# Optimization experiments

Measured on AMD Instinct MI355X. Metric: run time of the kernel, lower is better.

## Reference

```python
import math
import jax, jax.numpy as jnp
from jax import lax
import numpy as np

# Defaults of DifferenceOfGaussians
MIN_SIGMA, SIGMA_RATIO, MAX_SIGMA, TRUNCATE = 1.0, 1.2, 10.0, 4.0
K = int(np.log(MAX_SIGMA / MIN_SIGMA) / np.log(SIGMA_RATIO) + 1)  # 13
SIGMAS_NP = np.array([MIN_SIGMA * SIGMA_RATIO ** i for i in range(K + 1)], np.float32)
MAX_RADIUS = int(TRUNCATE * SIGMAS_NP.max() + 0.5)  # 43
THRESHOLD = 0.001
PAD = (3 - 1) // 2  # footprint=3 -> padding 1
MAX_PEAKS = 32768  # fixed cap for jit-compatible nonzero


def _build_pyramid_weight():
    """Replicates GaussianSmoothing kernels (incl. its exp(-(d/(2s))^2) form),
    zero-padded to the common 87x87 support. Shape [K+1, 1, 87, 87] (OIHW)."""
    ksz = 2 * MAX_RADIUS + 1
    W = np.zeros((K + 1, 1, ksz, ksz), np.float32)
    for i, s in enumerate(SIGMAS_NP):
        r = int(TRUNCATE * s + 0.5)
        n = 2 * r + 1
        g = np.arange(n, dtype=np.float32)
        mean = (n - 1) / 2.0
        g1 = (1.0 / (s * math.sqrt(2 * math.pi))) * np.exp(-(((g - mean) / (2.0 * s)) ** 2))
        k2 = np.outer(g1, g1)
        k2 /= k2.sum()
        p = MAX_RADIUS - r
        W[i, 0, p:p + n, p:p + n] = k2
    return jnp.asarray(W)


def setup_inputs() -> dict:
    key = jax.random.key(0)
    x = jax.random.uniform(key, (1, 1, 512, 512), dtype=jnp.float32)
    weight = _build_pyramid_weight()            # [14, 1, 87, 87]
    sigma_list = jnp.asarray(SIGMAS_NP)         # [14]
    return {"x": x, "weight": weight, "sigma_list": sigma_list}


def reference(x, weight, sigma_list):
    # ConstantPad2d(max_radius) then VALID conv -> output spatially == input
    xp = jnp.pad(x, ((0, 0), (0, 0), (MAX_RADIUS, MAX_RADIUS), (MAX_RADIUS, MAX_RADIUS)))
    g = lax.conv_general_dilated(
        xp, weight, window_strides=(1, 1), padding='VALID',
        dimension_numbers=('NCHW', 'OIHW', 'NCHW'))[0]        # [K+1, H, W]
    # DoG stack scaled by sigma: [K, H, W]
    dog = (g[:-1] - g[1:]) * sigma_list[:K][:, None, None]
    # 3D max-pool, kernel 3, stride 1, pad 1 (same shape)
    image_max = lax.reduce_window(dog, -jnp.inf, lax.max,
                                  (3, 3, 3), (1, 1, 1), [(PAD, PAD)] * 3)
    mask = (dog == image_max) & (dog > THRESHOLD)
    # exclude_border: zero out PAD-wide borders along every dim (incl. scale dim)
    mask = mask.at[:PAD].set(False).at[-PAD:].set(False)
    mask = mask.at[:, :PAD].set(False).at[:, -PAD:].set(False)
    mask = mask.at[:, :, :PAD].set(False).at[:, :, -PAD:].set(False)
    # fixed-size nonzero (padded rows have indices (0,0,0); (0,*,*) is always
    # masked out by border exclusion, so real peaks never collide with padding)
    s_idx, y_idx, x_idx = jnp.nonzero(mask, size=MAX_PEAKS, fill_value=0)
    local_maxima = jnp.stack([sigma_list[s_idx],
                              y_idx.astype(jnp.float32),
                              x_idx.astype(jnp.float32)], axis=1)  # [MAX_PEAKS, 3]
    return local_maxima
```

## Files before the change

kernel.cpp:

```cpp
#include <hip/hip_runtime.h>
#include <hip/hip_bf16.h>


#define OFF_H    0
#define OFF_DOG  18350080
#define OFF_BITS 31981568
#define OFF_GCNT 32407552

#define HROWS 640
#define HPAD  43
#define NSIG 13
#define MAXPEAKS 32768

__device__ __forceinline__ void make_w(float s, double sgn, double* wl, int lane) {
    int r = (int)(4.0f * s + 0.5f);
    int n = 2 * r + 1;
    double v0 = 0.0, v1 = 0.0;
    double sd = (double)s;
    if (lane < n) {
        double d = (double)(lane - r), q = d / (2.0 * sd);
        v0 = exp(-q * q);
    }
    if (lane + 64 < n) {
        double d = (double)(lane + 64 - r), q = d / (2.0 * sd);
        v1 = exp(-q * q);
    }
    double part = v0 + v1;
    for (int m = 1; m < 64; m <<= 1) part += __shfl_xor(part, m);
    double inv = sgn / part;
    wl[lane] = v0 * inv;
    if (lane + 64 < 96) wl[lane + 64] = v1 * inv;
}

__global__ __launch_bounds__(256) void hpass(const float* __restrict__ x,
                                             const float* __restrict__ sigma_list,
                                             float* __restrict__ h) {
    const int i = 13 - blockIdx.y;
    const int t = threadIdx.x;
    float s = sigma_list[i];
    int r = (int)(4.0f * s + 0.5f);
    int n = 2 * r + 1;
    int nceil = (n + 15) & ~15;

    __shared__ double wl[96];
    if (t < 64) make_w(s, +1.0, wl, t);

    {
        float* hp = h + i * (HROWS * 512);
        for (int k = t; k < 688; k += 256) {
            int f = blockIdx.x * 688 + k;
            int g = f >> 9, xc = f & 511;
            int row = (g < HPAD) ? g : (g + 512);
            hp[row * 512 + xc] = 0.0f;
        }
    }

    __shared__ float rowp[8][648];
    int y8 = blockIdx.x * 8;
    for (int rr = 0; rr < 8; ++rr)
        for (int k = t; k < 608; k += 256) {
            int gx = k - 43;
            float val = ((unsigned)gx < 512u) ? x[(y8 + rr) * 512 + gx] : 0.0f;
            rowp[rr][k + (k >> 4)] = val;
        }
    __syncthreads();

    int tsub = t & 31, row = t >> 5;
    int xb = tsub * 16;
    int P0 = 43 - r + xb;
    double acc[16], win[16];
#pragma unroll
    for (int j = 0; j < 16; ++j) acc[j] = 0.0;
#pragma unroll
    for (int sl = 0; sl < 16; ++sl) {
        int p = P0 + sl;
        win[sl] = (double)rowp[row][p + (p >> 4)];
    }
    for (int dc = 0; dc < nceil; dc += 16) {
#pragma unroll
        for (int k = 0; k < 16; ++k) {
            double wd = wl[dc + k];
#pragma unroll
            for (int j = 0; j < 16; ++j)
                acc[j] = fma(wd, win[(k + j) & 15], acc[j]);
            int p = P0 + dc + k + 16;
            win[k] = (double)rowp[row][p + (p >> 4)];
        }
    }
    float* hp = h + (i * HROWS + HPAD + y8 + row) * 512 + xb;
#pragma unroll
    for (int j = 0; j < 16; ++j) hp[j] = (float)acc[j];
}

__device__ __forceinline__ void conv_acc(const float* __restrict__ bp,
                                         int nceil, const double* __restrict__ wl,
                                         double (&acc)[16]) {
    double win[16];
#pragma unroll
    for (int sl = 0; sl < 16; ++sl) win[sl] = (double)bp[sl * 512];
    for (int dc = 0; dc < nceil; dc += 16) {
        const float* rp = bp + (dc + 16) * 512;
#pragma unroll
        for (int k = 0; k < 16; ++k) {
            double wd = wl[dc + k];
#pragma unroll
            for (int j = 0; j < 16; ++j)
                acc[j] = fma(wd, win[(k + j) & 15], acc[j]);
            win[k] = (double)rp[k * 512];
        }
    }
}

__global__ __launch_bounds__(64) void vdog(const float* __restrict__ h,
                                           const float* __restrict__ sigma_list,
                                           float* __restrict__ dog) {
    const int di = 12 - blockIdx.z;
    const int lane = threadIdx.x;
    const int x = blockIdx.x * 64 + lane;
    const int y0 = blockIdx.y * 16;
    float s0 = sigma_list[di], s1 = sigma_list[di + 1];
    int r0 = (int)(4.0f * s0 + 0.5f), n0 = 2 * r0 + 1, nc0 = (n0 + 15) & ~15;
    int r1 = (int)(4.0f * s1 + 0.5f), n1 = 2 * r1 + 1, nc1 = (n1 + 15) & ~15;
    __shared__ double wl0[96], wl1[96];
    make_w(s0, +1.0, wl0, lane);
    make_w(s1, -1.0, wl1, lane);
    __syncthreads();
    double acc[16];
#pragma unroll
    for (int j = 0; j < 16; ++j) acc[j] = 0.0;
    const float* hp0 = h + di * (HROWS * 512);
    conv_acc(hp0 + (HPAD + y0 - r0) * 512 + x, nc0, wl0, acc);
    const float* hp1 = hp0 + HROWS * 512;
    conv_acc(hp1 + (HPAD + y0 - r1) * 512 + x, nc1, wl1, acc);
    double sg = (double)s0;
    float* dp = dog + (di * 512 + y0) * 512 + x;
#pragma unroll
    for (int j = 0; j < 16; ++j) dp[j * 512] = (float)(acc[j] * sg);
}

__global__ __launch_bounds__(512) void detect(const float* __restrict__ dog,
                                              unsigned long long* __restrict__ rowbits,
                                              int* __restrict__ gcnt) {
    const int s = blockIdx.y;
    const int y0 = blockIdx.x * 8;
    const int group = s * 64 + blockIdx.x;
    const int t = threadIdx.x;
    const int w = t >> 6, lane = t & 63;

    if (s == 0 || s == 12) {
        if (t < 64) rowbits[(s * 512 + y0 + (t >> 3)) * 8 + (t & 7)] = 0ull;
        if (t == 0) gcnt[group] = 0;
        return;
    }

    float pm[10], vcen[8];
#pragma unroll
    for (int k = 0; k < 8; ++k) vcen[k] = 0.0f;
#pragma unroll
    for (int q = 0; q < 10; ++q) {
        int yy = y0 - 1 + q;
        float m = -3.0e38f;
        if ((unsigned)yy < 512u) {
            float a = dog[((s - 1) * 512 + yy) * 512 + t];
            float b = dog[(s * 512 + yy) * 512 + t];
            float c = dog[((s + 1) * 512 + yy) * 512 + t];
            m = fmaxf(a, fmaxf(b, c));
            if (q >= 1 && q <= 8) vcen[q - 1] = b;
        }
        pm[q] = m;
    }
    __shared__ float cml[8][512];
    __shared__ int cnt[8][8];
#pragma unroll
    for (int k = 0; k < 8; ++k)
        cml[k][t] = fmaxf(pm[k], fmaxf(pm[k + 1], pm[k + 2]));
    __syncthreads();
#pragma unroll
    for (int k = 0; k < 8; ++k) {
        int y = y0 + k;
        bool peak = false;
        if (t >= 1 && t <= 510 && y >= 1 && y <= 510) {
            float v = vcen[k];
            if (v > 0.001f) {
                float mx = fmaxf(cml[k][t - 1], fmaxf(cml[k][t], cml[k][t + 1]));
                peak = (v >= mx);
            }
        }
        unsigned long long m = __ballot(peak);
        if (lane == 0) {
            rowbits[(s * 512 + y) * 8 + w] = m;
            cnt[k][w] = __popcll(m);
        }
    }
    __syncthreads();
    if (t == 0) {
        int c = 0;
#pragma unroll
        for (int k = 0; k < 8; ++k)
#pragma unroll
            for (int q = 0; q < 8; ++q) c += cnt[k][q];
        gcnt[group] = c;
    }
}

__global__ __launch_bounds__(512) void emit(const unsigned long long* __restrict__ rowbits,
                                            const int* __restrict__ gcnt,
                                            const float* __restrict__ sigma_list,
                                            float* __restrict__ out) {
    const int b = blockIdx.x;
    const int s = b >> 6;
    const int y0 = (b & 63) * 8;
    const int t = threadIdx.x;
    const int lane = t & 63;

    __shared__ unsigned long long m[64];
    __shared__ int pre[64];
    __shared__ int redA[512], redB[512];

    if (t < 64) m[t] = rowbits[(s * 512 + y0 + (t >> 3)) * 8 + (t & 7)];

    int pa = 0, pb = 0;
    {
        int c0 = (t < 832) ? gcnt[t] : 0;
        int i1 = t + 512;
        int c1 = (i1 < 832) ? gcnt[i1] : 0;
        pb = c0 + c1;
        if (t < b) pa += c0;
        if (i1 < b) pa += c1;
    }
    redA[t] = pa;
    redB[t] = pb;
    __syncthreads();
    for (int off = 256; off > 0; off >>= 1) {
        if (t < off) { redA[t] += redA[t + off]; redB[t] += redB[t + off]; }
        __syncthreads();
    }
    int gbase = redA[0];
    int tot = min(redB[0], MAXPEAKS);

    if (t < 64) {
        int wc = (int)__popcll(m[t]);
        int inc = wc;
        for (int off = 1; off < 64; off <<= 1) {
            int v = __shfl_up(inc, off);
            if (lane >= off) inc += v;
        }
        pre[t] = inc - wc;
    }
    __syncthreads();

#pragma unroll
    for (int k = 0; k < 8; ++k) {
        int widx = k * 8 + (t >> 6);
        unsigned long long mw = m[widx];
        if ((mw >> lane) & 1ull) {
            int pos = gbase + pre[widx] + (int)__popcll(mw & ((1ull << lane) - 1ull));
            if (pos < MAXPEAKS) {
                out[pos * 3 + 0] = sigma_list[s];
                out[pos * 3 + 1] = (float)(y0 + k);
                out[pos * 3 + 2] = (float)t;
            }
        }
    }

    int idx = b * 512 + t;
    if (idx < MAXPEAKS && idx >= tot) {
        out[idx * 3 + 0] = sigma_list[0];
        out[idx * 3 + 1] = 0.0f;
        out[idx * 3 + 2] = 0.0f;
    }
}

extern "C" void kernel_launch(void* const* d_in, const int* in_sizes, int n_in,
                              void* d_out, int out_size, void* d_ws, size_t ws_size,
                              hipStream_t stream) {
    const float* x     = (const float*)d_in[0];
    const float* sigma = (const float*)d_in[2];
    float* out = (float*)d_out;

    char* ws = (char*)d_ws;
    float* h                     = (float*)(ws + OFF_H);
    float* dog                   = (float*)(ws + OFF_DOG);
    unsigned long long* rowbits  = (unsigned long long*)(ws + OFF_BITS);
    int* gcnt                    = (int*)(ws + OFF_GCNT);

    hpass<<<dim3(64, 14), 256, 0, stream>>>(x, sigma, h);
    vdog<<<dim3(8, 32, 13), 64, 0, stream>>>(h, sigma, dog);
    detect<<<dim3(64, 13), 512, 0, stream>>>(dog, rowbits, gcnt);
    emit<<<832, 512, 0, stream>>>(rowbits, gcnt, sigma, out);
}
```

Before: 110.7 us.

## Trim conv tap padding, fuse scale pairs in detect, and early-exit emit

Both separable convolution passes now round the tap count up to a multiple of 8 instead of 16, and handle the final 8 taps in a separate tail loop. This drops zero-weight FMAs on the fp64 accumulation path. The detect kernel now processes two adjacent scales per block and shares the loaded DoG planes between them, which cuts global reads and block count. The emit kernel returns early for blocks with no peaks and replaces its shared-memory tree reduction with wavefront shuffles, at the cost of more code paths and register pressure.

```diff
diff --git a/kernel.cpp b/kernel.cpp
--- a/kernel.cpp
+++ b/kernel.cpp
@@ -40,7 +40,7 @@
     float s = sigma_list[i];
     int r = (int)(4.0f * s + 0.5f);
     int n = 2 * r + 1;
-    int nceil = (n + 15) & ~15;
+    int nc8 = (n + 7) & ~7;
 
     __shared__ double wl[96];
     if (t < 64) make_w(s, +1.0, wl, t);
@@ -76,7 +76,8 @@
         int p = P0 + sl;
         win[sl] = (double)rowp[row][p + (p >> 4)];
     }
-    for (int dc = 0; dc < nceil; dc += 16) {
+    int full = nc8 & ~15;
+    for (int dc = 0; dc < full; dc += 16) {
 #pragma unroll
         for (int k = 0; k < 16; ++k) {
             double wd = wl[dc + k];
@@ -87,22 +88,45 @@
             win[k] = (double)rowp[row][p + (p >> 4)];
         }
     }
+    if (nc8 & 8) {
+#pragma unroll
+        for (int k = 0; k < 8; ++k) {
+            double wd = wl[full + k];
+#pragma unroll
+            for (int j = 0; j < 16; ++j)
+                acc[j] = fma(wd, win[(k + j) & 15], acc[j]);
+            int p = P0 + full + k + 16;
+            win[k] = (double)rowp[row][p + (p >> 4)];
+        }
+    }
     float* hp = h + (i * HROWS + HPAD + y8 + row) * 512 + xb;
 #pragma unroll
     for (int j = 0; j < 16; ++j) hp[j] = (float)acc[j];
 }
 
 __device__ __forceinline__ void conv_acc(const float* __restrict__ bp,
-                                         int nceil, const double* __restrict__ wl,
+                                         int nc8, const double* __restrict__ wl,
                                          double (&acc)[16]) {
     double win[16];
 #pragma unroll
     for (int sl = 0; sl < 16; ++sl) win[sl] = (double)bp[sl * 512];
-    for (int dc = 0; dc < nceil; dc += 16) {
+    int full = nc8 & ~15;
+    for (int dc = 0; dc < full; dc += 16) {
         const float* rp = bp + (dc + 16) * 512;
 #pragma unroll
         for (int k = 0; k < 16; ++k) {
             double wd = wl[dc + k];
+#pragma unroll
+            for (int j = 0; j < 16; ++j)
+                acc[j] = fma(wd, win[(k + j) & 15], acc[j]);
+            win[k] = (double)rp[k * 512];
+        }
+    }
+    if (nc8 & 8) {
+        const float* rp = bp + (full + 16) * 512;
+#pragma unroll
+        for (int k = 0; k < 8; ++k) {
+            double wd = wl[full + k];
 #pragma unroll
             for (int j = 0; j < 16; ++j)
                 acc[j] = fma(wd, win[(k + j) & 15], acc[j]);
@@ -119,8 +143,8 @@
     const int x = blockIdx.x * 64 + lane;
     const int y0 = blockIdx.y * 16;
     float s0 = sigma_list[di], s1 = sigma_list[di + 1];
-    int r0 = (int)(4.0f * s0 + 0.5f), n0 = 2 * r0 + 1, nc0 = (n0 + 15) & ~15;
-    int r1 = (int)(4.0f * s1 + 0.5f), n1 = 2 * r1 + 1, nc1 = (n1 + 15) & ~15;
+    int r0 = (int)(4.0f * s0 + 0.5f), n0 = 2 * r0 + 1, nc0 = (n0 + 7) & ~7;
+    int r1 = (int)(4.0f * s1 + 0.5f), n1 = 2 * r1 + 1, nc1 = (n1 + 7) & ~7;
     __shared__ double wl0[96], wl1[96];
     make_w(s0, +1.0, wl0, lane);
     make_w(s1, -1.0, wl1, lane);
@@ -141,55 +165,96 @@
 __global__ __launch_bounds__(512) void detect(const float* __restrict__ dog,
                                               unsigned long long* __restrict__ rowbits,
                                               int* __restrict__ gcnt) {
-    const int s = blockIdx.y;
-    const int y0 = blockIdx.x * 8;
-    const int group = s * 64 + blockIdx.x;
+    const int z = blockIdx.y;
+    const int sA = 2 * z + 1;
+    const bool hasB = (sA < 11);
+    const int bx = blockIdx.x;
+    const int y0 = bx * 8;
     const int t = threadIdx.x;
     const int w = t >> 6, lane = t & 63;
 
-    if (s == 0 || s == 12) {
-        if (t < 64) rowbits[(s * 512 + y0 + (t >> 3)) * 8 + (t & 7)] = 0ull;
-        if (t == 0) gcnt[group] = 0;
-        return;
-    }
-
-    float pm[10], vcen[8];
-#pragma unroll
-    for (int k = 0; k < 8; ++k) vcen[k] = 0.0f;
-#pragma unroll
-    for (int q = 0; q < 10; ++q) {
-        int yy = y0 - 1 + q;
-        float m = -3.0e38f;
-        if ((unsigned)yy < 512u) {
-            float a = dog[((s - 1) * 512 + yy) * 512 + t];
-            float b = dog[(s * 512 + yy) * 512 + t];
-            float c = dog[((s + 1) * 512 + yy) * 512 + t];
-            m = fmaxf(a, fmaxf(b, c));
-            if (q >= 1 && q <= 8) vcen[q - 1] = b;
-        }
-        pm[q] = m;
-    }
-    __shared__ float cml[8][512];
-    __shared__ int cnt[8][8];
-#pragma unroll
-    for (int k = 0; k < 8; ++k)
-        cml[k][t] = fmaxf(pm[k], fmaxf(pm[k + 1], pm[k + 2]));
-    __syncthreads();
+    if (z == 0) {
+        if (t < 64) rowbits[(0 * 512 + y0 + (t >> 3)) * 8 + (t & 7)] = 0ull;
+        if (t == 0) gcnt[0 * 64 + bx] = 0;
+    } else if (z == 5) {
+        if (t < 64) rowbits[(12 * 512 + y0 + (t >> 3)) * 8 + (t & 7)] = 0ull;
+        if (t == 0) gcnt[12 * 64 + bx] = 0;
+    }
+
+    const int p0 = sA - 1;
+    float rm[4][8];
+    float vA[8], vB[8];
+#pragma unroll
+    for (int pp = 0; pp < 4; ++pp) {
+        if (pp == 3 && !hasB) {
+#pragma unroll
+            for (int k = 0; k < 8; ++k) rm[3][k] = -3.0e38f;
+        } else {
+            const float* dp = dog + (p0 + pp) * (512 * 512) + t;
+            float val[10];
+#pragma unroll
+            for (int q = 0; q < 10; ++q) {
+                int yy = y0 - 1 + q;
+                val[q] = ((unsigned)yy < 512u) ? dp[yy * 512] : -3.0e38f;
+            }
+#pragma unroll
+            for (int k = 0; k < 8; ++k)
+                rm[pp][k] = fmaxf(val[k], fmaxf(val[k + 1], val[k + 2]));
+            if (pp == 1) {
+#pragma unroll
+                for (int k = 0; k < 8; ++k) vA[k] = val[k + 1];
+            }
+            if (pp == 2) {
+#pragma unroll
+                for (int k = 0; k < 8; ++k) vB[k] = val[k + 1];
+            }
+        }
+    }
+
+    __shared__ float cml[2][8][512];
+    __shared__ int cnt[2][8][8];
+#pragma unroll
+    for (int k = 0; k < 8; ++k) {
+        cml[0][k][t] = fmaxf(rm[0][k], fmaxf(rm[1][k], rm[2][k]));
+        cml[1][k][t] = fmaxf(rm[1][k], fmaxf(rm[2][k], rm[3][k]));
+    }
+    __syncthreads();
+
 #pragma unroll
     for (int k = 0; k < 8; ++k) {
         int y = y0 + k;
         bool peak = false;
         if (t >= 1 && t <= 510 && y >= 1 && y <= 510) {
-            float v = vcen[k];
+            float v = vA[k];
             if (v > 0.001f) {
-                float mx = fmaxf(cml[k][t - 1], fmaxf(cml[k][t], cml[k][t + 1]));
+                float mx = fmaxf(cml[0][k][t - 1], fmaxf(cml[0][k][t], cml[0][k][t + 1]));
                 peak = (v >= mx);
             }
         }
         unsigned long long m = __ballot(peak);
         if (lane == 0) {
-            rowbits[(s * 512 + y) * 8 + w] = m;
-            cnt[k][w] = __popcll(m);
+            rowbits[(sA * 512 + y) * 8 + w] = m;
+            cnt[0][k][w] = __popcll(m);
+        }
+    }
+    if (hasB) {
+        const int sB = sA + 1;
+#pragma unroll
+        for (int k = 0; k < 8; ++k) {
+            int y = y0 + k;
+            bool peak = false;
+            if (t >= 1 && t <= 510 && y >= 1 && y <= 510) {
+                float v = vB[k];
+                if (v > 0.001f) {
+                    float mx = fmaxf(cml[1][k][t - 1], fmaxf(cml[1][k][t], cml[1][k][t + 1]));
+                    peak = (v >= mx);
+                }
+            }
+            unsigned long long m = __ballot(peak);
+            if (lane == 0) {
+                rowbits[(sB * 512 + y) * 8 + w] = m;
+                cnt[1][k][w] = __popcll(m);
+            }
         }
     }
     __syncthreads();
@@ -198,8 +263,16 @@
 #pragma unroll
         for (int k = 0; k < 8; ++k)
 #pragma unroll
-            for (int q = 0; q < 8; ++q) c += cnt[k][q];
-        gcnt[group] = c;
+            for (int q = 0; q < 8; ++q) c += cnt[0][k][q];
+        gcnt[sA * 64 + bx] = c;
+        if (hasB) {
+            c = 0;
+#pragma unroll
+            for (int k = 0; k < 8; ++k)
+#pragma unroll
+                for (int q = 0; q < 8; ++q) c += cnt[1][k][q];
+            gcnt[(sA + 1) * 64 + bx] = c;
+        }
     }
 }
 
@@ -211,11 +284,13 @@
     const int s = b >> 6;
     const int y0 = (b & 63) * 8;
     const int t = threadIdx.x;
-    const int lane = t & 63;
+    const int w = t >> 6, lane = t & 63;
+
+    if (b >= 64 && gcnt[b] == 0) return;
 
     __shared__ unsigned long long m[64];
     __shared__ int pre[64];
-    __shared__ int redA[512], redB[512];
+    __shared__ int wsumA[8], wsumB[8];
 
     if (t < 64) m[t] = rowbits[(s * 512 + y0 + (t >> 3)) * 8 + (t & 7)];
 
@@ -228,15 +303,12 @@
         if (t < b) pa += c0;
         if (i1 < b) pa += c1;
     }
-    redA[t] = pa;
-    redB[t] = pb;
-    __syncthreads();
-    for (int off = 256; off > 0; off >>= 1) {
-        if (t < off) { redA[t] += redA[t + off]; redB[t] += redB[t + off]; }
-        __syncthreads();
-    }
-    int gbase = redA[0];
-    int tot = min(redB[0], MAXPEAKS);
+#pragma unroll
+    for (int off = 32; off > 0; off >>= 1) {
+        pa += __shfl_down(pa, off);
+        pb += __shfl_down(pb, off);
+    }
+    if (lane == 0) { wsumA[w] = pa; wsumB[w] = pb; }
 
     if (t < 64) {
         int wc = (int)__popcll(m[t]);
@@ -248,6 +320,11 @@
         pre[t] = inc - wc;
     }
     __syncthreads();
+
+    int gbase = 0, tot = 0;
+#pragma unroll
+    for (int i = 0; i < 8; ++i) { gbase += wsumA[i]; tot += wsumB[i]; }
+    tot = min(tot, MAXPEAKS);
 
 #pragma unroll
     for (int k = 0; k < 8; ++k) {
@@ -286,6 +363,6 @@
 
     hpass<<<dim3(64, 14), 256, 0, stream>>>(x, sigma, h);
     vdog<<<dim3(8, 32, 13), 64, 0, stream>>>(h, sigma, dog);
-    detect<<<dim3(64, 13), 512, 0, stream>>>(dog, rowbits, gcnt);
+    detect<<<dim3(64, 6), 512, 0, stream>>>(dog, rowbits, gcnt);
     emit<<<832, 512, 0, stream>>>(rowbits, gcnt, sigma, out);
 }
```

New measurement: 110.4 us, median of 2. Within noise of the previous version (-0.3%).
